# Kernel optimization log

Measured on AMD Instinct MI355X. Metric: run time of the kernel, lower is better.

The kernel has to match this reference:

```python
import jax, jax.numpy as jnp
import numpy as np

B, N, G = 32, 1024, 8   # batch, Nvecs (= k_in), Nglobals
K_OUT, H = 128, 128     # MLP output width, hidden width
D_IN = 1 + N + G        # MLP input width: [u, norm, dots]


def setup_inputs() -> dict:
    key = jax.random.key(0)
    ks = jax.random.split(key, 8)
    x = jax.random.uniform(ks[0], (B, N, 3), dtype=jnp.float32)  # positive coords -> dots >= 0
    u = jax.random.normal(ks[1], (B, G), dtype=jnp.float32)
    s0 = 1.0 / np.sqrt(D_IN)
    s1 = 1.0 / np.sqrt(H)
    W0 = jax.random.normal(ks[2], (D_IN, H), dtype=jnp.float32) * s0
    b0 = jnp.zeros((H,), dtype=jnp.float32)
    W1 = jax.random.normal(ks[3], (H, H), dtype=jnp.float32) * s1
    b1 = jnp.zeros((H,), dtype=jnp.float32)
    W2 = jax.random.normal(ks[4], (H, K_OUT), dtype=jnp.float32) * s1
    b2 = jnp.zeros((K_OUT,), dtype=jnp.float32)
    return {"x": x, "u": u, "W0": W0, "b0": b0, "W1": W1, "b1": b1, "W2": W2, "b2": b2}


def reference(x, u, W0, b0, W1, b1, W2, b2):
    # x: [B, N, 3], u: [B, G]
    norms = jnp.linalg.norm(x, axis=-1, keepdims=True)            # [B, N, 1]
    dots = jnp.sqrt(jnp.einsum('bid,bjd->bij', x, x))             # [B, N, N]
    u_rep = jnp.broadcast_to(u[:, None, :], (x.shape[0], x.shape[1], u.shape[-1]))
    scalars = jnp.concatenate([u_rep, norms, dots], axis=-1)      # [B, N, G+1+N]
    # MLP (Linear -> LeakyReLU -> Linear -> LeakyReLU -> Linear)
    h = jax.nn.leaky_relu(scalars @ W0 + b0)
    h = jax.nn.leaky_relu(h @ W1 + b1)
    fk = h @ W2 + b2                                              # [B, N, K_OUT]
    # outer product 'bio,bid->biod' followed by mean over i == fused contraction
    out = jnp.einsum('bio,bid->bod', fk, x) / x.shape[1]          # [B, K_OUT, 3]
    return out
```

## Files before the change

kernel.cpp:

```cpp
#include <hip/hip_runtime.h>
#include <hip/hip_fp16.h>

typedef _Float16 f16;
typedef f16 f16x4 __attribute__((ext_vector_type(4)));
typedef f16 f16x8 __attribute__((ext_vector_type(8)));
typedef float f32x4 __attribute__((ext_vector_type(4)));

#define NN 1024

#define IMG2_OFF  0
#define W8_OFF    327680
#define BIAS0_OFF 328192

__global__ __launch_bounds__(256) void prep_kernel(
    const float* __restrict__ u,  const float* __restrict__ W0,
    const float* __restrict__ b0, const float* __restrict__ W1,
    const float* __restrict__ W2,
    f16* __restrict__ img2, float* __restrict__ w8v, float* __restrict__ bias0,
    float* __restrict__ outp)
{
    const int t = threadIdx.x;
    const int blk = blockIdx.x;
    if (blk < 160) {
        int flat = blk * 1024 + t * 4;
        int c   = flat >> 13;
        int rem = flat & 8191;
        int s0  = rem & 7;
        int lm  = (rem >> 3) & 15;
        int q   = (rem >> 7) & 3;
        int ks  = (rem >> 9) & 1;
        int nt  = (rem >> 10) & 3;
        int wn  = (rem >> 12) & 1;
        int n = wn * 64 + nt * 16 + lm;
        f16x4 v;
#pragma unroll
        for (int e = 0; e < 4; ++e) {
            int k = ks * 32 + q * 8 + s0 + e;
            float val;
            if (c < 16)       val = W0[(9 + c * 64 + k) * 128 + n];
            else if (c < 18)  val = W1[((c - 16) * 64 + k) * 128 + n];
            else              val = W2[((c - 18) * 64 + k) * 128 + n];
            v[e] = (f16)val;
        }
        *(f16x4*)&img2[flat] = v;
    } else if (blk < 176) {
        int idx = (blk - 160) * 256 + t;
        int b = idx >> 7, h = idx & 127;
        float s = b0[h];
#pragma unroll
        for (int g = 0; g < 8; ++g) s += u[b * 8 + g] * W0[g * 128 + h];
        bias0[idx] = s;
    } else if (blk == 176) {
        if (t < 128) w8v[t] = W0[8 * 128 + t];
    } else {
        int idx = (blk - 177) * 1024 + t * 4;
        if (idx < 12288) { float4 z = {0.f, 0.f, 0.f, 0.f}; *(float4*)&outp[idx] = z; }
    }
}

__global__ __launch_bounds__(256, 2) void fused_kernel(
    const float* __restrict__ x, const float* __restrict__ b1p,
    const float* __restrict__ b2p, const f16* __restrict__ img2,
    const float* __restrict__ w8v, const float* __restrict__ bias0,
    float* __restrict__ outp)
{
    __shared__ __align__(16) f16 Dsh[2][64 * 128];
    __shared__ __align__(16) f16 xjsh[1024 * 4];
    __shared__ __align__(16) float xi[64 * 4];
    __shared__ float normv[64];
    __shared__ float biass[128];
    __shared__ float w8s[128];

    const int t = threadIdx.x;
    const int b = blockIdx.x >> 4;
    const int i0 = (blockIdx.x & 15) * 64;

    const int lane = t & 63, wv = t >> 6;
    const int lm = lane & 15, q = lane >> 4;
    const int half = wv >> 1;
    const int nbase = (wv & 1) * 2;
    f16* Hh = &Dsh[0][0];

    {
        const float* xb = x + (size_t)b * NN * 3;
        float4 v0 = *(const float4*)(xb + t * 12);
        float4 v1 = *(const float4*)(xb + t * 12 + 4);
        float4 v2 = *(const float4*)(xb + t * 12 + 8);
        f16x4 r0; r0[0] = (f16)v0.x; r0[1] = (f16)v0.y; r0[2] = (f16)v0.z; r0[3] = (f16)0;
        f16x4 r1; r1[0] = (f16)v0.w; r1[1] = (f16)v1.x; r1[2] = (f16)v1.y; r1[3] = (f16)0;
        f16x4 r2; r2[0] = (f16)v1.z; r2[1] = (f16)v1.w; r2[2] = (f16)v2.x; r2[3] = (f16)0;
        f16x4 r3; r3[0] = (f16)v2.y; r3[1] = (f16)v2.z; r3[2] = (f16)v2.w; r3[3] = (f16)0;
        *(f16x4*)&xjsh[(t * 4 + 0) * 4] = r0;
        *(f16x4*)&xjsh[(t * 4 + 1) * 4] = r1;
        *(f16x4*)&xjsh[(t * 4 + 2) * 4] = r2;
        *(f16x4*)&xjsh[(t * 4 + 3) * 4] = r3;
    }
    if (t < 192) {
        int i = t / 3, d = t - i * 3;
        xi[i * 4 + d] = x[(size_t)(b * NN + i0 + i) * 3 + d];
    }
    if (t < 128) { biass[t] = bias0[b * 128 + t]; w8s[t] = w8v[t]; }
    __syncthreads();
    if (t < 64) {
        float a0 = xi[t * 4], a1 = xi[t * 4 + 1], a2 = xi[t * 4 + 2];
        normv[t] = __builtin_amdgcn_sqrtf(a0 * a0 + a1 * a1 + a2 * a2);
    }

    f16x4 bi[4];
#pragma unroll
    for (int it = 0; it < 4; ++it) {
        f16x4 v; v[0] = (f16)0; v[1] = (f16)0; v[2] = (f16)0; v[3] = (f16)0;
        if (q == 0) {
            int ii = it * 16 + lm;
            v[0] = (f16)xi[ii * 4];
            v[1] = (f16)xi[ii * 4 + 1];
            v[2] = (f16)xi[ii * 4 + 2];
        }
        bi[it] = v;
    }

    auto dotstore = [&](int C, int buf) {
#pragma unroll
        for (int sub = 0; sub < 2; ++sub) {
            f16x4 ajv; ajv[0] = (f16)0; ajv[1] = (f16)0; ajv[2] = (f16)0; ajv[3] = (f16)0;
            if (q == 0)
                ajv = *(const f16x4*)&xjsh[(C * 128 + sub * 64 + wv * 16 + lm) * 4];
#pragma unroll
            for (int it = 0; it < 4; ++it) {
                f32x4 z; z[0] = 0.f; z[1] = 0.f; z[2] = 0.f; z[3] = 0.f;
                f32x4 cg = __builtin_amdgcn_mfma_f32_16x16x16f16(ajv, bi[it], z, 0, 0, 0);
                f16x4 dv;
#pragma unroll
                for (int r = 0; r < 4; ++r)
                    dv[r] = (f16)__builtin_amdgcn_sqrtf(fmaxf(cg[r], 0.f));
                int row = it * 16 + lm;
                int colstart = sub * 64 + wv * 16 + q * 4;
                int addr = row * 128 + (((colstart & ~7) ^ ((row & 7) << 3)) | (colstart & 7));
                *(f16x4*)&Dsh[buf][addr] = dv;
            }
        }
    };

    f32x4 acc[4][2];
    auto zero_acc = [&]() {
#pragma unroll
        for (int mt = 0; mt < 4; ++mt)
#pragma unroll
            for (int n2 = 0; n2 < 2; ++n2)
#pragma unroll
                for (int e = 0; e < 4; ++e) acc[mt][n2][e] = 0.f;
    };
    zero_acc();

    f16x8 bfbuf[2][2][4];
    auto loadB = [&](int C, int par) {
#pragma unroll
        for (int sub = 0; sub < 2; ++sub) {
            const f16* wb = img2 + (size_t)((2 * C + sub) * 2 + half) * 4096 + lane * 8;
#pragma unroll
            for (int n2 = 0; n2 < 2; ++n2)
#pragma unroll
                for (int ks = 0; ks < 2; ++ks)
                    bfbuf[par][n2][sub * 2 + ks] =
                        *(const f16x8*)(wb + ((nbase + n2) * 2 + ks) * 512);
        }
    };

    loadB(0, 0);
    dotstore(0, 0);
    __syncthreads();

#pragma unroll
    for (int jc = 0; jc < 8; ++jc) {
        const int cur = jc & 1, nxt = cur ^ 1;
        if (jc < 7) loadB(jc + 1, nxt);
        f16x8 af[4][4];
#pragma unroll
        for (int mt = 0; mt < 4; ++mt)
#pragma unroll
            for (int kk = 0; kk < 4; ++kk) {
                int row = mt * 16 + lm;
                int col = kk * 32 + q * 8;
                af[mt][kk] = *(const f16x8*)(Dsh[cur] + row * 128 + (col ^ ((row & 7) << 3)));
            }
        if (jc < 7) dotstore(jc + 1, nxt);
#pragma unroll
        for (int kk = 0; kk < 4; ++kk)
#pragma unroll
            for (int mt = 0; mt < 4; ++mt)
#pragma unroll
                for (int n2 = 0; n2 < 2; ++n2)
                    acc[mt][n2] = __builtin_amdgcn_mfma_f32_16x16x32_f16(
                        af[mt][kk], bfbuf[cur][n2][kk], acc[mt][n2], 0, 0, 0);
        __syncthreads();
    }

    f16x8 bL[2][4];
#pragma unroll
    for (int n2 = 0; n2 < 2; ++n2)
#pragma unroll
        for (int kk = 0; kk < 4; ++kk) {
            const f16* wb = img2 + (size_t)((16 + (kk >> 1)) * 2 + half) * 4096 + lane * 8;
            bL[n2][kk] = *(const f16x8*)(wb + ((nbase + n2) * 2 + (kk & 1)) * 512);
        }

#pragma unroll
    for (int mt = 0; mt < 4; ++mt)
#pragma unroll
        for (int n2 = 0; n2 < 2; ++n2) {
            const int h = wv * 32 + n2 * 16 + lm;
            const float bh = biass[h], w8h = w8s[h];
#pragma unroll
            for (int r = 0; r < 4; ++r) {
                int i = mt * 16 + q * 4 + r;
                float val = acc[mt][n2][r] + bh + normv[i] * w8h;
                val = val > 0.f ? val : 0.01f * val;
                int addr = i * 128 + (((h & ~7) ^ ((i & 7) << 3)) | (h & 7));
                Hh[addr] = (f16)val;
            }
        }
    __syncthreads();

    zero_acc();
#pragma unroll
    for (int kk = 0; kk < 4; ++kk) {
        f16x8 af[4];
#pragma unroll
        for (int mt = 0; mt < 4; ++mt) {
            int row = mt * 16 + lm;
            int col = kk * 32 + q * 8;
            af[mt] = *(const f16x8*)(Hh + row * 128 + (col ^ ((row & 7) << 3)));
        }
#pragma unroll
        for (int mt = 0; mt < 4; ++mt)
#pragma unroll
            for (int n2 = 0; n2 < 2; ++n2)
                acc[mt][n2] = __builtin_amdgcn_mfma_f32_16x16x32_f16(
                    af[mt], bL[n2][kk], acc[mt][n2], 0, 0, 0);
    }

    f16x8 bM[2][4];
#pragma unroll
    for (int n2 = 0; n2 < 2; ++n2)
#pragma unroll
        for (int kk = 0; kk < 4; ++kk) {
            const f16* wb = img2 + (size_t)((18 + (kk >> 1)) * 2 + half) * 4096 + lane * 8;
            bM[n2][kk] = *(const f16x8*)(wb + ((nbase + n2) * 2 + (kk & 1)) * 512);
        }
    __syncthreads();

#pragma unroll
    for (int mt = 0; mt < 4; ++mt)
#pragma unroll
        for (int n2 = 0; n2 < 2; ++n2) {
            const int h = wv * 32 + n2 * 16 + lm;
            const float bh = b1p[h];
#pragma unroll
            for (int r = 0; r < 4; ++r) {
                int i = mt * 16 + q * 4 + r;
                float val = acc[mt][n2][r] + bh;
                val = val > 0.f ? val : 0.01f * val;
                int addr = i * 128 + (((h & ~7) ^ ((i & 7) << 3)) | (h & 7));
                Hh[addr] = (f16)val;
            }
        }
    __syncthreads();

    zero_acc();
#pragma unroll
    for (int kk = 0; kk < 4; ++kk) {
        f16x8 af[4];
#pragma unroll
        for (int mt = 0; mt < 4; ++mt) {
            int row = mt * 16 + lm;
            int col = kk * 32 + q * 8;
            af[mt] = *(const f16x8*)(Hh + row * 128 + (col ^ ((row & 7) << 3)));
        }
#pragma unroll
        for (int mt = 0; mt < 4; ++mt)
#pragma unroll
            for (int n2 = 0; n2 < 2; ++n2)
                acc[mt][n2] = __builtin_amdgcn_mfma_f32_16x16x32_f16(
                    af[mt], bM[n2][kk], acc[mt][n2], 0, 0, 0);
    }

    float p[2][3];
#pragma unroll
    for (int n2 = 0; n2 < 2; ++n2)
#pragma unroll
        for (int d = 0; d < 3; ++d) p[n2][d] = 0.f;
    float bo[2];
#pragma unroll
    for (int n2 = 0; n2 < 2; ++n2) bo[n2] = b2p[wv * 32 + n2 * 16 + lm];
#pragma unroll
    for (int mt = 0; mt < 4; ++mt)
#pragma unroll
        for (int r = 0; r < 4; ++r) {
            int i = mt * 16 + q * 4 + r;
            float x0 = xi[i * 4], x1 = xi[i * 4 + 1], x2 = xi[i * 4 + 2];
#pragma unroll
            for (int n2 = 0; n2 < 2; ++n2) {
                float fkv = acc[mt][n2][r] + bo[n2];
                p[n2][0] = fmaf(fkv, x0, p[n2][0]);
                p[n2][1] = fmaf(fkv, x1, p[n2][1]);
                p[n2][2] = fmaf(fkv, x2, p[n2][2]);
            }
        }
#pragma unroll
    for (int n2 = 0; n2 < 2; ++n2)
#pragma unroll
        for (int d = 0; d < 3; ++d) {
            float s = p[n2][d];
            s += __shfl_xor(s, 16);
            s += __shfl_xor(s, 32);
            if (q == 0) {
                int o = wv * 32 + n2 * 16 + lm;
                atomicAdd(&outp[(b * 128 + o) * 3 + d], s * (1.0f / 1024.0f));
            }
        }
}

extern "C" void kernel_launch(void* const* d_in, const int* in_sizes, int n_in,
                              void* d_out, int out_size, void* d_ws, size_t ws_size,
                              hipStream_t stream) {
    const float* x  = (const float*)d_in[0];
    const float* u  = (const float*)d_in[1];
    const float* W0 = (const float*)d_in[2];
    const float* b0 = (const float*)d_in[3];
    const float* W1 = (const float*)d_in[4];
    const float* b1 = (const float*)d_in[5];
    const float* W2 = (const float*)d_in[6];
    const float* b2 = (const float*)d_in[7];

    char* ws = (char*)d_ws;
    f16*   img2  = (f16*)(ws + IMG2_OFF);
    float* w8v   = (float*)(ws + W8_OFF);
    float* bias0 = (float*)(ws + BIAS0_OFF);
    float* out   = (float*)d_out;

    prep_kernel<<<189, 256, 0, stream>>>(u, W0, b0, W1, W2, img2, w8v, bias0, out);
    fused_kernel<<<512, 256, 0, stream>>>(x, b1, b2, img2, w8v, bias0, out);
}
```

Measured before the change: 87.43 us.

## Spill dots tile to global fragment image, then stream it for layer-0 GEMM

The fused kernel now builds the 64x1024 sqrt-dot tile in 64-column chunks through a smaller LDS double buffer and writes it to a per-block global scratch image laid out in MFMA fragment order. The layer-0 GEMM then streams A fragments from that global image with register double buffering, so the main loop no longer needs LDS barriers, and launch bounds move to 3 blocks per CU. The aim is to decouple dot generation from the GEMM and raise occupancy. In exchange it adds about 64 MB of global write and read traffic and forces a serialized write-then-read phase.

```diff
diff --git a/kernel.cpp b/kernel.cpp
--- a/kernel.cpp
+++ b/kernel.cpp
@@ -11,6 +11,7 @@
 #define IMG2_OFF  0
 #define W8_OFF    327680
 #define BIAS0_OFF 328192
+#define DIMG_OFF  1048576
 
 __global__ __launch_bounds__(256) void prep_kernel(
     const float* __restrict__ u,  const float* __restrict__ W0,
@@ -58,13 +59,13 @@
     }
 }
 
-__global__ __launch_bounds__(256, 2) void fused_kernel(
+__global__ __launch_bounds__(256, 3) void fused_kernel(
     const float* __restrict__ x, const float* __restrict__ b1p,
     const float* __restrict__ b2p, const f16* __restrict__ img2,
     const float* __restrict__ w8v, const float* __restrict__ bias0,
-    float* __restrict__ outp)
+    f16* __restrict__ Dimg, float* __restrict__ outp)
 {
-    __shared__ __align__(16) f16 Dsh[2][64 * 128];
+    __shared__ __align__(16) f16 Dsh[2][64 * 64];
     __shared__ __align__(16) f16 xjsh[1024 * 4];
     __shared__ __align__(16) float xi[64 * 4];
     __shared__ float normv[64];
@@ -80,6 +81,7 @@
     const int half = wv >> 1;
     const int nbase = (wv & 1) * 2;
     f16* Hh = &Dsh[0][0];
+    f16* Dg = Dimg + (size_t)blockIdx.x * 65536;
 
     {
         const float* xb = x + (size_t)b * NN * 3;
@@ -119,27 +121,41 @@
         bi[it] = v;
     }
 
-    auto dotstore = [&](int C, int buf) {
-#pragma unroll
-        for (int sub = 0; sub < 2; ++sub) {
-            f16x4 ajv; ajv[0] = (f16)0; ajv[1] = (f16)0; ajv[2] = (f16)0; ajv[3] = (f16)0;
-            if (q == 0)
-                ajv = *(const f16x4*)&xjsh[(C * 128 + sub * 64 + wv * 16 + lm) * 4];
-#pragma unroll
-            for (int it = 0; it < 4; ++it) {
-                f32x4 z; z[0] = 0.f; z[1] = 0.f; z[2] = 0.f; z[3] = 0.f;
-                f32x4 cg = __builtin_amdgcn_mfma_f32_16x16x16f16(ajv, bi[it], z, 0, 0, 0);
-                f16x4 dv;
-#pragma unroll
-                for (int r = 0; r < 4; ++r)
-                    dv[r] = (f16)__builtin_amdgcn_sqrtf(fmaxf(cg[r], 0.f));
-                int row = it * 16 + lm;
-                int colstart = sub * 64 + wv * 16 + q * 4;
-                int addr = row * 128 + (((colstart & ~7) ^ ((row & 7) << 3)) | (colstart & 7));
-                *(f16x4*)&Dsh[buf][addr] = dv;
-            }
+    auto dotstore = [&](int jc, int buf) {
+        f16x4 ajv; ajv[0] = (f16)0; ajv[1] = (f16)0; ajv[2] = (f16)0; ajv[3] = (f16)0;
+        if (q == 0)
+            ajv = *(const f16x4*)&xjsh[(jc * 64 + wv * 16 + lm) * 4];
+#pragma unroll
+        for (int it = 0; it < 4; ++it) {
+            f32x4 z; z[0] = 0.f; z[1] = 0.f; z[2] = 0.f; z[3] = 0.f;
+            f32x4 cg = __builtin_amdgcn_mfma_f32_16x16x16f16(ajv, bi[it], z, 0, 0, 0);
+            f16x4 dv;
+#pragma unroll
+            for (int r = 0; r < 4; ++r)
+                dv[r] = (f16)__builtin_amdgcn_sqrtf(fmaxf(cg[r], 0.f));
+            int row = it * 16 + lm;
+            int colstart = wv * 16 + q * 4;
+            int addr = row * 64 + (((colstart & ~7) ^ ((row & 7) << 3)) | (colstart & 7));
+            *(f16x4*)&Dsh[buf][addr] = dv;
         }
     };
+
+    dotstore(0, 0);
+    __syncthreads();
+#pragma unroll 4
+    for (int jc = 0; jc < 16; ++jc) {
+        const int cur = jc & 1, nxt = cur ^ 1;
+        if (jc < 15) dotstore(jc + 1, nxt);
+#pragma unroll
+        for (int ks = 0; ks < 2; ++ks) {
+            int row = wv * 16 + lm;
+            int col = ks * 32 + q * 8;
+            f16x8 v = *(const f16x8*)(Dsh[cur] + row * 64 + (col ^ ((row & 7) << 3)));
+            *(f16x8*)(Dg + ((size_t)(jc * 8 + wv * 2 + ks) * 64 + lane) * 8) = v;
+        }
+        __syncthreads();
+    }
+    __syncthreads();
 
     f32x4 acc[4][2];
     auto zero_acc = [&]() {
@@ -152,47 +168,35 @@
     };
     zero_acc();
 
-    f16x8 bfbuf[2][2][4];
-    auto loadB = [&](int C, int par) {
-#pragma unroll
-        for (int sub = 0; sub < 2; ++sub) {
-            const f16* wb = img2 + (size_t)((2 * C + sub) * 2 + half) * 4096 + lane * 8;
-#pragma unroll
-            for (int n2 = 0; n2 < 2; ++n2)
-#pragma unroll
-                for (int ks = 0; ks < 2; ++ks)
-                    bfbuf[par][n2][sub * 2 + ks] =
-                        *(const f16x8*)(wb + ((nbase + n2) * 2 + ks) * 512);
-        }
+    f16x8 afb[2][8];
+    f16x8 bfbuf[2][2][2];
+    auto loadA = [&](int jc, int par) {
+#pragma unroll
+        for (int f = 0; f < 8; ++f)
+            afb[par][f] = *(const f16x8*)(Dg + ((size_t)(jc * 8 + f) * 64 + lane) * 8);
     };
-
+    auto loadB = [&](int jc, int par) {
+        const f16* wb = img2 + (size_t)(jc * 2 + half) * 4096 + lane * 8;
+#pragma unroll
+        for (int n2 = 0; n2 < 2; ++n2)
+#pragma unroll
+            for (int ks = 0; ks < 2; ++ks)
+                bfbuf[par][n2][ks] = *(const f16x8*)(wb + ((nbase + n2) * 2 + ks) * 512);
+    };
+    loadA(0, 0);
     loadB(0, 0);
-    dotstore(0, 0);
-    __syncthreads();
-
-#pragma unroll
-    for (int jc = 0; jc < 8; ++jc) {
+#pragma unroll 2
+    for (int jc = 0; jc < 16; ++jc) {
         const int cur = jc & 1, nxt = cur ^ 1;
-        if (jc < 7) loadB(jc + 1, nxt);
-        f16x8 af[4][4];
-#pragma unroll
-        for (int mt = 0; mt < 4; ++mt)
-#pragma unroll
-            for (int kk = 0; kk < 4; ++kk) {
-                int row = mt * 16 + lm;
-                int col = kk * 32 + q * 8;
-                af[mt][kk] = *(const f16x8*)(Dsh[cur] + row * 128 + (col ^ ((row & 7) << 3)));
-            }
-        if (jc < 7) dotstore(jc + 1, nxt);
-#pragma unroll
-        for (int kk = 0; kk < 4; ++kk)
+        if (jc < 15) { loadA(jc + 1, nxt); loadB(jc + 1, nxt); }
+#pragma unroll
+        for (int ks = 0; ks < 2; ++ks)
 #pragma unroll
             for (int mt = 0; mt < 4; ++mt)
 #pragma unroll
                 for (int n2 = 0; n2 < 2; ++n2)
                     acc[mt][n2] = __builtin_amdgcn_mfma_f32_16x16x32_f16(
-                        af[mt][kk], bfbuf[cur][n2][kk], acc[mt][n2], 0, 0, 0);
-        __syncthreads();
+                        afb[cur][mt * 2 + ks], bfbuf[cur][n2][ks], acc[mt][n2], 0, 0, 0);
     }
 
     f16x8 bL[2][4];
@@ -336,8 +340,9 @@
     f16*   img2  = (f16*)(ws + IMG2_OFF);
     float* w8v   = (float*)(ws + W8_OFF);
     float* bias0 = (float*)(ws + BIAS0_OFF);
+    f16*   Dimg  = (f16*)(ws + DIMG_OFF);
     float* out   = (float*)d_out;
 
     prep_kernel<<<189, 256, 0, stream>>>(u, W0, b0, W1, W2, img2, w8v, bias0, out);
-    fused_kernel<<<512, 256, 0, stream>>>(x, b1, b2, img2, w8v, bias0, out);
+    fused_kernel<<<512, 256, 0, stream>>>(x, b1, b2, img2, w8v, bias0, Dimg, out);
 }
```

After: 210.0 us. 2.4x slower.
